# Kernel tuning notes

Hardware: AMD Instinct MI355X
Metric: run time of the kernel (lower is better)

The kernel has to match this reference:

```python
import jax, jax.numpy as jnp
import numpy as np

K_CODES, D_DIM = 512, 64


def setup_inputs() -> dict:
    key = jax.random.key(0)
    k1, k2 = jax.random.split(key)
    x = jax.random.normal(k1, (32, D_DIM, 64, 64), dtype=jnp.float32)  # NCHW
    weight = jax.random.uniform(k2, (K_CODES, D_DIM), minval=-1.0 / K_CODES,
                                maxval=1.0 / K_CODES, dtype=jnp.float32)
    return {"x": x, "weight": weight}


def reference(x, weight):
    K = weight.shape[0]
    xp = jnp.transpose(x, (0, 2, 3, 1))          # [B, H, W, D]
    flat = xp.reshape(-1, weight.shape[1])       # [N, D]
    dist = (jnp.sum(flat * flat, axis=1, keepdims=True)
            + jnp.sum(weight * weight, axis=1)
            - 2.0 * flat @ weight.T)
    idx = jnp.argmin(dist, axis=1)               # [N]
    enc = jax.nn.one_hot(idx, K, dtype=jnp.float32)   # [N, K] one-hot scatter
    quantized = (enc @ weight).reshape(xp.shape)      # matmul codebook lookup
    commit_loss = jnp.mean(jnp.square(jax.lax.stop_gradient(quantized) - xp))
    vq_loss = jnp.mean(jnp.square(quantized - jax.lax.stop_gradient(xp)))
    loss = vq_loss + 1.0 * commit_loss           # commitment_cost = 1.0
    quant_st = xp + jax.lax.stop_gradient(quantized - xp)  # straight-through
    return (loss, jnp.transpose(quant_st, (0, 3, 1, 2)), enc, idx)
```

## Files before the change

kernel.cpp:

```cpp
#include <hip/hip_runtime.h>
#include <cfloat>

#define KC 512
#define DD 64
#define HW 4096
#define NPIX 131072
#define QSIZE 8388608
#define PXB 128
#define NBLK (NPIX / PXB)
#define NTH 512
#define MARGIN 4.0e-3f

typedef short short8 __attribute__((ext_vector_type(8)));
typedef float f32x4 __attribute__((ext_vector_type(4)));
typedef float nfloat4 __attribute__((ext_vector_type(4)));
typedef unsigned long long u64;

__device__ __forceinline__ unsigned short bf16_rne(float f) {
    unsigned int u = __float_as_uint(f);
    u += 0x7FFFu + ((u >> 16) & 1u);
    return (unsigned short)(u >> 16);
}

__global__ __launch_bounds__(1024) void prep(
    const float* __restrict__ w, float* __restrict__ w2g,
    uint4* __restrict__ wswz) {
  const int gt = blockIdx.x * 1024 + threadIdx.x;
  {
    int ct = gt >> 7, kc = (gt >> 6) & 1, ln = gt & 63;
    int n = ln & 15, q = ln >> 4;
    const float* wp = w + (ct * 16 + n) * DD + kc * 32 + q * 8;
    nfloat4 f0 = *(const nfloat4*)(wp);
    nfloat4 f1 = *(const nfloat4*)(wp + 4);
    uint4 u;
    u.x = (unsigned)bf16_rne(f0[0]) | ((unsigned)bf16_rne(f0[1]) << 16);
    u.y = (unsigned)bf16_rne(f0[2]) | ((unsigned)bf16_rne(f0[3]) << 16);
    u.z = (unsigned)bf16_rne(f1[0]) | ((unsigned)bf16_rne(f1[1]) << 16);
    u.w = (unsigned)bf16_rne(f1[2]) | ((unsigned)bf16_rne(f1[3]) << 16);
    wswz[gt] = u;
  }
  if (gt < KC) {
    const float* wk = w + gt * DD;
    float r0 = __fmul_rn(wk[0], wk[0]), r1 = __fmul_rn(wk[1], wk[1]),
          r2 = __fmul_rn(wk[2], wk[2]), r3 = __fmul_rn(wk[3], wk[3]),
          r4 = __fmul_rn(wk[4], wk[4]), r5 = __fmul_rn(wk[5], wk[5]),
          r6 = __fmul_rn(wk[6], wk[6]), r7 = __fmul_rn(wk[7], wk[7]);
    #pragma unroll
    for (int i = 8; i < DD; i += 8) {
      r0 = __fadd_rn(r0, __fmul_rn(wk[i+0], wk[i+0]));
      r1 = __fadd_rn(r1, __fmul_rn(wk[i+1], wk[i+1]));
      r2 = __fadd_rn(r2, __fmul_rn(wk[i+2], wk[i+2]));
      r3 = __fadd_rn(r3, __fmul_rn(wk[i+3], wk[i+3]));
      r4 = __fadd_rn(r4, __fmul_rn(wk[i+4], wk[i+4]));
      r5 = __fadd_rn(r5, __fmul_rn(wk[i+5], wk[i+5]));
      r6 = __fadd_rn(r6, __fmul_rn(wk[i+6], wk[i+6]));
      r7 = __fadd_rn(r7, __fmul_rn(wk[i+7], wk[i+7]));
    }
    w2g[gt] = __fadd_rn(__fadd_rn(__fadd_rn(r0, r1), __fadd_rn(r2, r3)),
                        __fadd_rn(__fadd_rn(r4, r5), __fadd_rn(r6, r7)));
  }
}

__global__ __launch_bounds__(NTH, 4) void vq_fused(
    const float* __restrict__ x, const float* __restrict__ w,
    const float* __restrict__ w2g, const uint4* __restrict__ wswz,
    float* __restrict__ out_q, float* __restrict__ out_enc,
    float* __restrict__ out_idx, double* __restrict__ partial) {

  __shared__ uint4 wlds[4096];
  __shared__ float w2s[KC];
  __shared__ u64 candm[PXB][8];
  __shared__ float Xs[PXB];
  __shared__ int sidx[PXB];
  __shared__ float sredf[8];

  const int tid = threadIdx.x;
  const int lane = tid & 63;
  const int wv = tid >> 6;
  const int bix = blockIdx.x;
  const int b = bix >> 5;
  const int p0 = (bix & 31) * PXB;
  const float* xt = x + (size_t)b * (DD * HW) + p0;

  #pragma unroll
  for (int s = 0; s < 8; ++s) wlds[tid + s * NTH] = wswz[tid + s * NTH];
  w2s[tid] = w2g[tid];
  if (tid < KC - NTH) w2s[tid + NTH] = w2g[tid + NTH];
  for (int i = tid; i < PXB * 8; i += NTH) ((u64*)candm)[i] = 0;

  if (tid < PXB) {
    const float* xp = xt + tid;
    float r0 = __fmul_rn(xp[0*HW], xp[0*HW]), r1 = __fmul_rn(xp[1*HW], xp[1*HW]),
          r2 = __fmul_rn(xp[2*HW], xp[2*HW]), r3 = __fmul_rn(xp[3*HW], xp[3*HW]),
          r4 = __fmul_rn(xp[4*HW], xp[4*HW]), r5 = __fmul_rn(xp[5*HW], xp[5*HW]),
          r6 = __fmul_rn(xp[6*HW], xp[6*HW]), r7 = __fmul_rn(xp[7*HW], xp[7*HW]);
    #pragma unroll
    for (int i = 8; i < DD; i += 8) {
      r0 = __fadd_rn(r0, __fmul_rn(xp[(size_t)(i+0)*HW], xp[(size_t)(i+0)*HW]));
      r1 = __fadd_rn(r1, __fmul_rn(xp[(size_t)(i+1)*HW], xp[(size_t)(i+1)*HW]));
      r2 = __fadd_rn(r2, __fmul_rn(xp[(size_t)(i+2)*HW], xp[(size_t)(i+2)*HW]));
      r3 = __fadd_rn(r3, __fmul_rn(xp[(size_t)(i+3)*HW], xp[(size_t)(i+3)*HW]));
      r4 = __fadd_rn(r4, __fmul_rn(xp[(size_t)(i+4)*HW], xp[(size_t)(i+4)*HW]));
      r5 = __fadd_rn(r5, __fmul_rn(xp[(size_t)(i+5)*HW], xp[(size_t)(i+5)*HW]));
      r6 = __fadd_rn(r6, __fmul_rn(xp[(size_t)(i+6)*HW], xp[(size_t)(i+6)*HW]));
      r7 = __fadd_rn(r7, __fmul_rn(xp[(size_t)(i+7)*HW], xp[(size_t)(i+7)*HW]));
    }
    Xs[tid] = __fadd_rn(__fadd_rn(__fadd_rn(r0, r1), __fadd_rn(r2, r3)),
                        __fadd_rn(__fadd_rn(r4, r5), __fadd_rn(r6, r7)));
  }

  const int am = lane & 15, aq = lane >> 4;
  const float* xa = xt + wv * 16 + am;
  short8 a0, a1;
  #pragma unroll
  for (int j = 0; j < 8; ++j) {
    a0[j] = (short)bf16_rne(-2.0f * xa[(size_t)(aq * 8 + j) * HW]);
    a1[j] = (short)bf16_rne(-2.0f * xa[(size_t)(32 + aq * 8 + j) * HW]);
  }

  __syncthreads();

  const short8* wl8 = (const short8*)wlds;
  const int cn = lane & 15;

  float m0 = FLT_MAX, m1 = FLT_MAX, m2 = FLT_MAX, m3 = FLT_MAX;
  for (int ct = 0; ct < 32; ++ct) {
    float wk2 = w2s[ct * 16 + cn];
    f32x4 acc = {wk2, wk2, wk2, wk2};
    acc = __builtin_amdgcn_mfma_f32_16x16x32_bf16(a0, wl8[ct * 128 + lane], acc, 0, 0, 0);
    acc = __builtin_amdgcn_mfma_f32_16x16x32_bf16(a1, wl8[ct * 128 + 64 + lane], acc, 0, 0, 0);
    m0 = fminf(m0, acc[0]); m1 = fminf(m1, acc[1]);
    m2 = fminf(m2, acc[2]); m3 = fminf(m3, acc[3]);
  }
  #pragma unroll
  for (int s = 1; s < 16; s <<= 1) {
    m0 = fminf(m0, __shfl_xor(m0, s));
    m1 = fminf(m1, __shfl_xor(m1, s));
    m2 = fminf(m2, __shfl_xor(m2, s));
    m3 = fminf(m3, __shfl_xor(m3, s));
  }
  const float t0 = m0 + MARGIN, t1 = m1 + MARGIN,
              t2 = m2 + MARGIN, t3 = m3 + MARGIN;

  for (int ct = 0; ct < 32; ++ct) {
    float wk2 = w2s[ct * 16 + cn];
    f32x4 acc = {wk2, wk2, wk2, wk2};
    acc = __builtin_amdgcn_mfma_f32_16x16x32_bf16(a0, wl8[ct * 128 + lane], acc, 0, 0, 0);
    acc = __builtin_amdgcn_mfma_f32_16x16x32_bf16(a1, wl8[ct * 128 + 64 + lane], acc, 0, 0, 0);
    u64 bm0 = __ballot(acc[0] <= t0);
    u64 bm1 = __ballot(acc[1] <= t1);
    u64 bm2 = __ballot(acc[2] <= t2);
    u64 bm3 = __ballot(acc[3] <= t3);
    if (lane < 4) {
      u64 mk = (lane == 0) ? bm0 : (lane == 1) ? bm1 : (lane == 2) ? bm2 : bm3;
      int word = ct >> 2, sh = (ct & 3) * 16;
      #pragma unroll
      for (int q = 0; q < 4; ++q) {
        u64 bits = (mk >> (q * 16)) & 0xFFFFull;
        if (bits) candm[wv * 16 + q * 4 + lane][word] |= bits << sh;
      }
    }
  }
  __syncthreads();

  {
    const int px = tid >> 2, part = tid & 3;
    const float X = Xs[px];
    const float* xr = xt + px;
    float bestd = FLT_MAX; int bk = 1 << 30;
    for (int wd = part * 2; wd < part * 2 + 2; ++wd) {
      u64 msk = candm[px][wd];
      while (msk) {
        int bit = __ffsll((unsigned long long)msk) - 1;
        msk &= msk - 1;
        int k = wd * 64 + bit;
        const float* wp = w + k * DD;
        float P = 0.f;
        #pragma unroll
        for (int dc = 0; dc < 16; ++dc) {
          nfloat4 w4 = *(const nfloat4*)(wp + dc * 4);
          P = __fmaf_rn(xr[(size_t)(dc * 4 + 0) * HW], w4[0], P);
          P = __fmaf_rn(xr[(size_t)(dc * 4 + 1) * HW], w4[1], P);
          P = __fmaf_rn(xr[(size_t)(dc * 4 + 2) * HW], w4[2], P);
          P = __fmaf_rn(xr[(size_t)(dc * 4 + 3) * HW], w4[3], P);
        }
        float dist = __fsub_rn(__fadd_rn(X, w2s[k]), __fadd_rn(P, P));
        if (dist < bestd || (dist == bestd && k < bk)) { bestd = dist; bk = k; }
      }
    }
    float od = __shfl_down(bestd, 1); int ok = __shfl_down(bk, 1);
    if ((lane & 3) < 3 && (od < bestd || (od == bestd && ok < bk))) { bestd = od; bk = ok; }
    od = __shfl_down(bestd, 2); ok = __shfl_down(bk, 2);
    if ((lane & 3) < 2 && (od < bestd || (od == bestd && ok < bk))) { bestd = od; bk = ok; }
    if (part == 0) {
      sidx[px] = bk;
      out_idx[bix * PXB + px] = (float)bk;
    }
  }
  __syncthreads();

  float lsum = 0.f;
  float* qb = out_q + (size_t)b * (DD * HW) + p0;
  for (int i = tid; i < PXB * DD; i += NTH) {
    int d = i >> 7, pp = i & 127;
    float qv = w[sidx[pp] * DD + d];
    float dv = qv - xt[(size_t)d * HW + pp];
    lsum = __fmaf_rn(dv, dv, lsum);
    __builtin_nontemporal_store(qv, qb + (size_t)d * HW + pp);
  }
  #pragma unroll
  for (int off = 32; off > 0; off >>= 1) lsum += __shfl_down(lsum, off);
  if (lane == 0) sredf[wv] = lsum;
  __syncthreads();
  if (tid == 0) {
    double t = 0.0;
    #pragma unroll
    for (int i = 0; i < 8; ++i) t += (double)sredf[i];
    partial[bix] = t;
  }

  float* basep = out_enc + (size_t)bix * (PXB * KC);
  for (int t = tid; t < 16383; t += NTH) {
    int u = 3 + 4 * t;
    nfloat4 v;
    #pragma unroll
    for (int j = 0; j < 4; ++j) {
      int e = u + j;
      v[j] = (sidx[e >> 9] == (e & 511)) ? 1.0f : 0.0f;
    }
    __builtin_nontemporal_store(v, (nfloat4*)(basep + u));
  }
  if (tid < 3) basep[tid] = (sidx[0] == tid) ? 1.0f : 0.0f;
  else if (tid == 3) basep[PXB * KC - 1] = (sidx[127] == 511) ? 1.0f : 0.0f;
}

__global__ void finish_kernel(const double* __restrict__ partial,
                              float* __restrict__ out) {
  int t = threadIdx.x;
  double s = partial[t] + partial[t + 256] + partial[t + 512] + partial[t + 768];
  #pragma unroll
  for (int off = 32; off > 0; off >>= 1) s += __shfl_down(s, off);
  __shared__ double sr[4];
  if ((t & 63) == 0) sr[t >> 6] = s;
  __syncthreads();
  if (t == 0)
    out[0] = (float)(2.0 * (sr[0] + sr[1] + sr[2] + sr[3]) / (double)QSIZE);
}

extern "C" void kernel_launch(void* const* d_in, const int* in_sizes, int n_in,
                              void* d_out, int out_size, void* d_ws, size_t ws_size,
                              hipStream_t stream) {
  const float* x = (const float*)d_in[0];
  const float* w = (const float*)d_in[1];
  float* out = (float*)d_out;
  float* out_q = out + 1;
  float* out_enc = out_q + QSIZE;
  float* out_idx = out_enc + (size_t)NPIX * KC;

  double* partial = (double*)d_ws;
  float* w2g = (float*)((char*)d_ws + 8192);
  uint4* wswz = (uint4*)((char*)d_ws + 16384);

  prep<<<4, 1024, 0, stream>>>(w, w2g, wswz);
  vq_fused<<<NBLK, NTH, 0, stream>>>(x, w, w2g, wswz, out_q, out_enc, out_idx, partial);
  finish_kernel<<<1, 256, 0, stream>>>(partial, out);
}
```

Measured before the change: 384.4 us.

## Read bf16 codebook from global/L2 instead of LDS, raise occupancy, lighten barriers

The kernel no longer stages the 64KB swizzled bf16 codebook into shared memory. MFMA operands are now read straight from global memory, where they should hit L1/L2. This frees most of the LDS, so launch bounds allow 8 blocks per CU instead of 4. Full __syncthreads are replaced with LDS-only waitcnt barriers, and the loss-partial barrier moves after the one-hot writes so it no longer sits in front of them. The risk is higher per-iteration load latency from global reads in the distance loops.

```diff
diff --git a/kernel.cpp b/kernel.cpp
--- a/kernel.cpp
+++ b/kernel.cpp
@@ -20,6 +20,12 @@
     unsigned int u = __float_as_uint(f);
     u += 0x7FFFu + ((u >> 16) & 1u);
     return (unsigned short)(u >> 16);
+}
+
+__device__ __forceinline__ void barrier_lds_only() {
+    asm volatile("s_waitcnt lgkmcnt(0)" ::: "memory");
+    __builtin_amdgcn_s_barrier();
+    __builtin_amdgcn_sched_barrier(0);
 }
 
 __global__ __launch_bounds__(1024) void prep(
@@ -61,13 +67,12 @@
   }
 }
 
-__global__ __launch_bounds__(NTH, 4) void vq_fused(
+__global__ __launch_bounds__(NTH, 8) void vq_fused(
     const float* __restrict__ x, const float* __restrict__ w,
-    const float* __restrict__ w2g, const uint4* __restrict__ wswz,
+    const float* __restrict__ w2g, const short8* __restrict__ wsw8,
     float* __restrict__ out_q, float* __restrict__ out_enc,
     float* __restrict__ out_idx, double* __restrict__ partial) {
 
-  __shared__ uint4 wlds[4096];
   __shared__ float w2s[KC];
   __shared__ u64 candm[PXB][8];
   __shared__ float Xs[PXB];
@@ -77,16 +82,15 @@
   const int tid = threadIdx.x;
   const int lane = tid & 63;
   const int wv = tid >> 6;
+  const int cn = lane & 15;
   const int bix = blockIdx.x;
   const int b = bix >> 5;
   const int p0 = (bix & 31) * PXB;
   const float* xt = x + (size_t)b * (DD * HW) + p0;
 
-  #pragma unroll
-  for (int s = 0; s < 8; ++s) wlds[tid + s * NTH] = wswz[tid + s * NTH];
   w2s[tid] = w2g[tid];
-  if (tid < KC - NTH) w2s[tid + NTH] = w2g[tid + NTH];
-  for (int i = tid; i < PXB * 8; i += NTH) ((u64*)candm)[i] = 0;
+  ((u64*)candm)[tid] = 0;
+  ((u64*)candm)[tid + NTH] = 0;
 
   if (tid < PXB) {
     const float* xp = xt + tid;
@@ -120,15 +124,14 @@
 
   __syncthreads();
 
-  const short8* wl8 = (const short8*)wlds;
-  const int cn = lane & 15;
-
   float m0 = FLT_MAX, m1 = FLT_MAX, m2 = FLT_MAX, m3 = FLT_MAX;
   for (int ct = 0; ct < 32; ++ct) {
     float wk2 = w2s[ct * 16 + cn];
+    short8 b0 = wsw8[ct * 128 + lane];
+    short8 b1 = wsw8[ct * 128 + 64 + lane];
     f32x4 acc = {wk2, wk2, wk2, wk2};
-    acc = __builtin_amdgcn_mfma_f32_16x16x32_bf16(a0, wl8[ct * 128 + lane], acc, 0, 0, 0);
-    acc = __builtin_amdgcn_mfma_f32_16x16x32_bf16(a1, wl8[ct * 128 + 64 + lane], acc, 0, 0, 0);
+    acc = __builtin_amdgcn_mfma_f32_16x16x32_bf16(a0, b0, acc, 0, 0, 0);
+    acc = __builtin_amdgcn_mfma_f32_16x16x32_bf16(a1, b1, acc, 0, 0, 0);
     m0 = fminf(m0, acc[0]); m1 = fminf(m1, acc[1]);
     m2 = fminf(m2, acc[2]); m3 = fminf(m3, acc[3]);
   }
@@ -144,9 +147,11 @@
 
   for (int ct = 0; ct < 32; ++ct) {
     float wk2 = w2s[ct * 16 + cn];
+    short8 b0 = wsw8[ct * 128 + lane];
+    short8 b1 = wsw8[ct * 128 + 64 + lane];
     f32x4 acc = {wk2, wk2, wk2, wk2};
-    acc = __builtin_amdgcn_mfma_f32_16x16x32_bf16(a0, wl8[ct * 128 + lane], acc, 0, 0, 0);
-    acc = __builtin_amdgcn_mfma_f32_16x16x32_bf16(a1, wl8[ct * 128 + 64 + lane], acc, 0, 0, 0);
+    acc = __builtin_amdgcn_mfma_f32_16x16x32_bf16(a0, b0, acc, 0, 0, 0);
+    acc = __builtin_amdgcn_mfma_f32_16x16x32_bf16(a1, b1, acc, 0, 0, 0);
     u64 bm0 = __ballot(acc[0] <= t0);
     u64 bm1 = __ballot(acc[1] <= t1);
     u64 bm2 = __ballot(acc[2] <= t2);
@@ -161,7 +166,7 @@
       }
     }
   }
-  __syncthreads();
+  barrier_lds_only();
 
   {
     const int px = tid >> 2, part = tid & 3;
@@ -197,7 +202,7 @@
       out_idx[bix * PXB + px] = (float)bk;
     }
   }
-  __syncthreads();
+  barrier_lds_only();
 
   float lsum = 0.f;
   float* qb = out_q + (size_t)b * (DD * HW) + p0;
@@ -211,13 +216,6 @@
   #pragma unroll
   for (int off = 32; off > 0; off >>= 1) lsum += __shfl_down(lsum, off);
   if (lane == 0) sredf[wv] = lsum;
-  __syncthreads();
-  if (tid == 0) {
-    double t = 0.0;
-    #pragma unroll
-    for (int i = 0; i < 8; ++i) t += (double)sredf[i];
-    partial[bix] = t;
-  }
 
   float* basep = out_enc + (size_t)bix * (PXB * KC);
   for (int t = tid; t < 16383; t += NTH) {
@@ -232,6 +230,14 @@
   }
   if (tid < 3) basep[tid] = (sidx[0] == tid) ? 1.0f : 0.0f;
   else if (tid == 3) basep[PXB * KC - 1] = (sidx[127] == 511) ? 1.0f : 0.0f;
+
+  barrier_lds_only();
+  if (tid == 0) {
+    double t = 0.0;
+    #pragma unroll
+    for (int i = 0; i < 8; ++i) t += (double)sredf[i];
+    partial[bix] = t;
+  }
 }
 
 __global__ void finish_kernel(const double* __restrict__ partial,
@@ -262,6 +268,7 @@
   uint4* wswz = (uint4*)((char*)d_ws + 16384);
 
   prep<<<4, 1024, 0, stream>>>(w, w2g, wswz);
-  vq_fused<<<NBLK, NTH, 0, stream>>>(x, w, w2g, wswz, out_q, out_enc, out_idx, partial);
+  vq_fused<<<NBLK, NTH, 0, stream>>>(x, w, w2g, (const short8*)wswz,
+                                     out_q, out_enc, out_idx, partial);
   finish_kernel<<<1, 256, 0, stream>>>(partial, out);
 }
```

After: 464.1 us. +20.7%, slower.

## Process two pixel tiles per block with per-wave independent work and no block barriers

Applied to the files above, without the earlier changes.

Halves the grid so each block loads the bf16 codebook into LDS once and then processes two 128-pixel tiles. Each wave now handles only its own 16 pixels end to end (norms, candidate masks, refinement, quantized output, one-hot rows, loss partial), so the block-wide __syncthreads are replaced with wave-local lgkmcnt waits. Loss partials become per-wave doubles, which enlarges the workspace and makes the finish kernel sum 8192 entries. This amortises the codebook staging and removes barrier stalls, at the cost of fewer blocks in flight and less parallelism for the tail.

```diff
diff --git a/kernel.cpp b/kernel.cpp
--- a/kernel.cpp
+++ b/kernel.cpp
@@ -7,7 +7,8 @@
 #define NPIX 131072
 #define QSIZE 8388608
 #define PXB 128
-#define NBLK (NPIX / PXB)
+#define NTILE (NPIX / PXB)
+#define NBLK (NTILE / 2)
 #define NTH 512
 #define MARGIN 4.0e-3f
 
@@ -20,6 +21,10 @@
     unsigned int u = __float_as_uint(f);
     u += 0x7FFFu + ((u >> 16) & 1u);
     return (unsigned short)(u >> 16);
+}
+
+__device__ __forceinline__ void wave_fence() {
+    asm volatile("s_waitcnt lgkmcnt(0)" ::: "memory");
 }
 
 __global__ __launch_bounds__(1024) void prep(
@@ -61,35 +66,21 @@
   }
 }
 
-__global__ __launch_bounds__(NTH, 4) void vq_fused(
-    const float* __restrict__ x, const float* __restrict__ w,
-    const float* __restrict__ w2g, const uint4* __restrict__ wswz,
-    float* __restrict__ out_q, float* __restrict__ out_enc,
-    float* __restrict__ out_idx, double* __restrict__ partial) {
-
-  __shared__ uint4 wlds[4096];
-  __shared__ float w2s[KC];
-  __shared__ u64 candm[PXB][8];
-  __shared__ float Xs[PXB];
-  __shared__ int sidx[PXB];
-  __shared__ float sredf[8];
-
-  const int tid = threadIdx.x;
-  const int lane = tid & 63;
-  const int wv = tid >> 6;
-  const int bix = blockIdx.x;
-  const int b = bix >> 5;
-  const int p0 = (bix & 31) * PXB;
-  const float* xt = x + (size_t)b * (DD * HW) + p0;
-
-  #pragma unroll
-  for (int s = 0; s < 8; ++s) wlds[tid + s * NTH] = wswz[tid + s * NTH];
-  w2s[tid] = w2g[tid];
-  if (tid < KC - NTH) w2s[tid + NTH] = w2g[tid + NTH];
-  for (int i = tid; i < PXB * 8; i += NTH) ((u64*)candm)[i] = 0;
-
-  if (tid < PXB) {
-    const float* xp = xt + tid;
+__device__ __forceinline__ void wave_tile(
+    const float* __restrict__ xt, const float* __restrict__ w,
+    const float* w2s, const short8* wl8,
+    u64 (*candm)[8], float* Xs, int* sidx,
+    float* __restrict__ qb, float* __restrict__ bp,
+    float* __restrict__ out_idx, double* __restrict__ partial,
+    int bix, int lane, int wv) {
+
+  {
+    u64* cz = (u64*)(candm + wv * 16);
+    cz[lane] = 0;
+    cz[lane + 64] = 0;
+  }
+  if (lane < 16) {
+    const float* xp = xt + wv * 16 + lane;
     float r0 = __fmul_rn(xp[0*HW], xp[0*HW]), r1 = __fmul_rn(xp[1*HW], xp[1*HW]),
           r2 = __fmul_rn(xp[2*HW], xp[2*HW]), r3 = __fmul_rn(xp[3*HW], xp[3*HW]),
           r4 = __fmul_rn(xp[4*HW], xp[4*HW]), r5 = __fmul_rn(xp[5*HW], xp[5*HW]),
@@ -105,10 +96,10 @@
       r6 = __fadd_rn(r6, __fmul_rn(xp[(size_t)(i+6)*HW], xp[(size_t)(i+6)*HW]));
       r7 = __fadd_rn(r7, __fmul_rn(xp[(size_t)(i+7)*HW], xp[(size_t)(i+7)*HW]));
     }
-    Xs[tid] = __fadd_rn(__fadd_rn(__fadd_rn(r0, r1), __fadd_rn(r2, r3)),
-                        __fadd_rn(__fadd_rn(r4, r5), __fadd_rn(r6, r7)));
-  }
-
+    Xs[wv * 16 + lane] =
+        __fadd_rn(__fadd_rn(__fadd_rn(r0, r1), __fadd_rn(r2, r3)),
+                  __fadd_rn(__fadd_rn(r4, r5), __fadd_rn(r6, r7)));
+  }
   const int am = lane & 15, aq = lane >> 4;
   const float* xa = xt + wv * 16 + am;
   short8 a0, a1;
@@ -117,10 +108,8 @@
     a0[j] = (short)bf16_rne(-2.0f * xa[(size_t)(aq * 8 + j) * HW]);
     a1[j] = (short)bf16_rne(-2.0f * xa[(size_t)(32 + aq * 8 + j) * HW]);
   }
-
-  __syncthreads();
-
-  const short8* wl8 = (const short8*)wlds;
+  wave_fence();
+
   const int cn = lane & 15;
 
   float m0 = FLT_MAX, m1 = FLT_MAX, m2 = FLT_MAX, m3 = FLT_MAX;
@@ -161,10 +150,10 @@
       }
     }
   }
-  __syncthreads();
+  wave_fence();
 
   {
-    const int px = tid >> 2, part = tid & 3;
+    const int px = wv * 16 + (lane >> 2), part = lane & 3;
     const float X = Xs[px];
     const float* xr = xt + px;
     float bestd = FLT_MAX; int bk = 1 << 30;
@@ -197,47 +186,88 @@
       out_idx[bix * PXB + px] = (float)bk;
     }
   }
-  __syncthreads();
-
+  wave_fence();
+
+  const int ppl = wv * 16 + (lane & 15);
+  const int kk = sidx[ppl];
+  const int dbase = lane >> 4;
   float lsum = 0.f;
-  float* qb = out_q + (size_t)b * (DD * HW) + p0;
-  for (int i = tid; i < PXB * DD; i += NTH) {
-    int d = i >> 7, pp = i & 127;
-    float qv = w[sidx[pp] * DD + d];
-    float dv = qv - xt[(size_t)d * HW + pp];
+  #pragma unroll
+  for (int it = 0; it < 16; ++it) {
+    int d = dbase + it * 4;
+    float qv = w[kk * DD + d];
+    float dv = qv - xt[(size_t)d * HW + ppl];
     lsum = __fmaf_rn(dv, dv, lsum);
-    __builtin_nontemporal_store(qv, qb + (size_t)d * HW + pp);
-  }
-  #pragma unroll
-  for (int off = 32; off > 0; off >>= 1) lsum += __shfl_down(lsum, off);
-  if (lane == 0) sredf[wv] = lsum;
-  __syncthreads();
-  if (tid == 0) {
-    double t = 0.0;
-    #pragma unroll
-    for (int i = 0; i < 8; ++i) t += (double)sredf[i];
-    partial[bix] = t;
-  }
-
-  float* basep = out_enc + (size_t)bix * (PXB * KC);
-  for (int t = tid; t < 16383; t += NTH) {
+    __builtin_nontemporal_store(qv, qb + (size_t)d * HW + ppl);
+  }
+
+  for (int t = lane; t < 2047; t += 64) {
     int u = 3 + 4 * t;
+    int e = wv * 8192 + u;
     nfloat4 v;
     #pragma unroll
     for (int j = 0; j < 4; ++j) {
-      int e = u + j;
-      v[j] = (sidx[e >> 9] == (e & 511)) ? 1.0f : 0.0f;
-    }
-    __builtin_nontemporal_store(v, (nfloat4*)(basep + u));
-  }
-  if (tid < 3) basep[tid] = (sidx[0] == tid) ? 1.0f : 0.0f;
-  else if (tid == 3) basep[PXB * KC - 1] = (sidx[127] == 511) ? 1.0f : 0.0f;
+      int ej = e + j;
+      v[j] = (sidx[ej >> 9] == (ej & 511)) ? 1.0f : 0.0f;
+    }
+    __builtin_nontemporal_store(v, (nfloat4*)(bp + u));
+  }
+  if (lane < 3) bp[lane] = (sidx[wv * 16] == lane) ? 1.0f : 0.0f;
+  else if (lane == 3) bp[8191] = (sidx[wv * 16 + 15] == 511) ? 1.0f : 0.0f;
+
+  #pragma unroll
+  for (int off = 32; off > 0; off >>= 1) lsum += __shfl_down(lsum, off);
+  if (lane == 0) partial[bix * 8 + wv] = (double)lsum;
+}
+
+__global__ __launch_bounds__(NTH, 4) void vq_fused(
+    const float* __restrict__ x, const float* __restrict__ w,
+    const float* __restrict__ w2g, const uint4* __restrict__ wswz,
+    float* __restrict__ out_q, float* __restrict__ out_enc,
+    float* __restrict__ out_idx, double* __restrict__ partial) {
+
+  __shared__ uint4 wlds[4096];
+  __shared__ float w2s[KC];
+  __shared__ u64 candm[PXB][8];
+  __shared__ float Xs[PXB];
+  __shared__ int sidx[PXB];
+
+  const int tid = threadIdx.x;
+  const int lane = tid & 63;
+  const int wv = tid >> 6;
+
+  const int bix0 = blockIdx.x;
+  const int b0 = bix0 >> 5;
+  const int q0 = (bix0 & 31) * PXB;
+  const float* xt0 = x + (size_t)b0 * (DD * HW) + q0;
+  const int bix1 = blockIdx.x + NBLK;
+  const int b1 = bix1 >> 5;
+  const int q1 = (bix1 & 31) * PXB;
+  const float* xt1 = x + (size_t)b1 * (DD * HW) + q1;
+
+  #pragma unroll
+  for (int s = 0; s < 8; ++s) wlds[tid + s * NTH] = wswz[tid + s * NTH];
+  w2s[tid] = w2g[tid];
+  __syncthreads();
+
+  const short8* wl8 = (const short8*)wlds;
+
+  wave_tile(xt0, w, w2s, wl8, candm, Xs, sidx,
+            out_q + (size_t)b0 * (DD * HW) + q0,
+            out_enc + (size_t)bix0 * (PXB * KC) + wv * 8192,
+            out_idx, partial, bix0, lane, wv);
+  wave_tile(xt1, w, w2s, wl8, candm, Xs, sidx,
+            out_q + (size_t)b1 * (DD * HW) + q1,
+            out_enc + (size_t)bix1 * (PXB * KC) + wv * 8192,
+            out_idx, partial, bix1, lane, wv);
 }
 
 __global__ void finish_kernel(const double* __restrict__ partial,
                               float* __restrict__ out) {
   int t = threadIdx.x;
-  double s = partial[t] + partial[t + 256] + partial[t + 512] + partial[t + 768];
+  double s = 0.0;
+  #pragma unroll
+  for (int i = 0; i < 32; ++i) s += partial[t + 256 * i];
   #pragma unroll
   for (int off = 32; off > 0; off >>= 1) s += __shfl_down(s, off);
   __shared__ double sr[4];
@@ -258,8 +288,8 @@
   float* out_idx = out_enc + (size_t)NPIX * KC;
 
   double* partial = (double*)d_ws;
-  float* w2g = (float*)((char*)d_ws + 8192);
-  uint4* wswz = (uint4*)((char*)d_ws + 16384);
+  float* w2g = (float*)((char*)d_ws + 65536);
+  uint4* wswz = (uint4*)((char*)d_ws + 69632);
 
   prep<<<4, 1024, 0, stream>>>(w, w2g, wswz);
   vq_fused<<<NBLK, NTH, 0, stream>>>(x, w, w2g, wswz, out_q, out_enc, out_idx, partial);
```

New measurement: 403.7 us. +5.0%, slower.
